# Performance work log

Measured on AMD Instinct MI355X. Metric: run time of the kernel, lower is better.

## Reference

```python
import jax, jax.numpy as jnp
import numpy as np

NEG_SLOPE = 0.2  # PyG GATv2Conv default negative_slope
HEADS1, HID, HEADS2, OUT = 8, 32, 1, 64


def gatv2_layer(x, src, dst, Wl, Wr, att, bias, heads, out_ch, concat):
    """One GATv2Conv (eval mode). x:[N,F], src/dst:[E], Wl/Wr:[F,heads*out_ch], att:[heads,out_ch]."""
    N = x.shape[0]
    xl = (x @ Wl).reshape(N, heads, out_ch)  # source-side transform (lin_l)
    xr = (x @ Wr).reshape(N, heads, out_ch)  # target-side transform (lin_r)
    z = xl[src] + xr[dst]                    # [E, H, C] per-edge pre-activation
    e = jnp.einsum('ehc,hc->eh', jax.nn.leaky_relu(z, NEG_SLOPE), att)  # [E, H]
    # numerically stable edge-softmax segmented by destination node
    m = jax.ops.segment_max(e, dst, num_segments=N)          # [N, H]
    a = jnp.exp(e - m[dst])
    s = jax.ops.segment_sum(a, dst, num_segments=N)          # [N, H]
    alpha = a / s[dst]                                       # [E, H]
    out = jax.ops.segment_sum(alpha[:, :, None] * xl[src], dst, num_segments=N)  # [N, H, C]
    out = out.reshape(N, heads * out_ch) if concat else out.mean(axis=1)
    return out + bias


def setup_inputs() -> dict:
    key = jax.random.key(0)
    ks = jax.random.split(key, 12)
    N, E, F_IN = 50000, 800000, 128
    x = jax.random.normal(ks[0], (N, F_IN), dtype=jnp.float32)
    edge_index = jax.random.randint(ks[1], (2, E), 0, N, dtype=jnp.int32)
    edge_type = jax.random.randint(ks[2], (E,), 0, 5, dtype=jnp.int32)
    sc = 0.05
    Wl1 = jax.random.normal(ks[3], (F_IN, HEADS1 * HID), dtype=jnp.float32) * sc
    Wr1 = jax.random.normal(ks[4], (F_IN, HEADS1 * HID), dtype=jnp.float32) * sc
    att1 = jax.random.normal(ks[5], (HEADS1, HID), dtype=jnp.float32) * sc
    b1 = jnp.zeros((HEADS1 * HID,), dtype=jnp.float32)
    Wl2 = jax.random.normal(ks[6], (HEADS1 * HID, HEADS2 * OUT), dtype=jnp.float32) * sc
    Wr2 = jax.random.normal(ks[7], (HEADS1 * HID, HEADS2 * OUT), dtype=jnp.float32) * sc
    att2 = jax.random.normal(ks[8], (HEADS2, OUT), dtype=jnp.float32) * sc
    b2 = jnp.zeros((OUT,), dtype=jnp.float32)
    return {"x": x, "edge_index": edge_index, "edge_type": edge_type,
            "Wl1": Wl1, "Wr1": Wr1, "att1": att1, "b1": b1,
            "Wl2": Wl2, "Wr2": Wr2, "att2": att2, "b2": b2}


def reference(x, edge_index, edge_type, Wl1, Wr1, att1, b1, Wl2, Wr2, att2, b2):
    # eval mode: F.dropout is identity; edge_type is unused by the original forward
    N = x.shape[0]
    loop = jnp.arange(N, dtype=edge_index.dtype)  # add_self_loops=True (PyG default)
    src = jnp.concatenate([edge_index[0], loop])
    dst = jnp.concatenate([edge_index[1], loop])
    h = jax.nn.elu(gatv2_layer(x, src, dst, Wl1, Wr1, att1, b1, HEADS1, HID, True))
    return gatv2_layer(h, src, dst, Wl2, Wr2, att2, b2, HEADS2, OUT, False)
```

## Files before the change

kernel.cpp:

```cpp
#include <hip/hip_runtime.h>
#include <math.h>

__device__ __forceinline__ float elu1(float z)  { return z > 0.f ? z : (__expf(z) - 1.f); }

__device__ __forceinline__ ushort f2b(float f) {
    uint u = __float_as_uint(f);
    uint r = (u + 0x7FFFu + ((u >> 16) & 1u)) >> 16;
    return (ushort)r;
}
__device__ __forceinline__ float b2f(ushort h) { return __uint_as_float(((uint)h) << 16); }
__device__ __forceinline__ float b2f_lo(uint u) { return __uint_as_float(u << 16); }
__device__ __forceinline__ float b2f_hi(uint u) { return __uint_as_float(u & 0xFFFF0000u); }

typedef __attribute__((ext_vector_type(8))) short short8b;
typedef __attribute__((ext_vector_type(4))) float f32x4;
typedef __attribute__((ext_vector_type(2))) float floatx2;

#define SCAN_BPB 1024


__global__ void k_hist(const int* __restrict__ ei, int E, int Et, int* __restrict__ deg) {
    int i = blockIdx.x * blockDim.x + threadIdx.x;
    if (i < Et) {
        int d = (i < E) ? ei[E + i] : (i - E);
        atomicAdd(&deg[d], 1);
    }
}


__global__ __launch_bounds__(256) void k_scan1(const int* __restrict__ deg, int N,
                                               int* __restrict__ bsum) {
    __shared__ int ts[256];
    int b = blockIdx.x, tid = threadIdx.x;
    int base = b * SCAN_BPB + tid * 4;
    int s = 0;
    if (base + 3 < N) {
        int4 v = *(const int4*)(deg + base);
        s = v.x + v.y + v.z + v.w;
    } else {
        for (int i = 0; i < 4; i++) if (base + i < N) s += deg[base + i];
    }
    ts[tid] = s;
    __syncthreads();
    for (int ofs = 128; ofs > 0; ofs >>= 1) {
        if (tid < ofs) ts[tid] += ts[tid + ofs];
        __syncthreads();
    }
    if (tid == 0) bsum[b] = ts[0];
}

__global__ __launch_bounds__(256) void k_scan2(int* __restrict__ bsum, int nb,
                                               int* __restrict__ offsets, int N) {
    __shared__ int sums[256];
    int tid = threadIdx.x;
    int v = (tid < nb) ? bsum[tid] : 0;
    sums[tid] = v;
    __syncthreads();
    for (int ofs = 1; ofs < 256; ofs <<= 1) {
        int t = 0;
        if (tid >= ofs) t = sums[tid - ofs];
        __syncthreads();
        sums[tid] += t;
        __syncthreads();
    }
    if (tid < nb) bsum[tid] = sums[tid] - v;
    if (tid == 255) offsets[N] = sums[255];
}

__global__ __launch_bounds__(256) void k_scan3(const int* __restrict__ deg, int N,
                                               const int* __restrict__ bsum,
                                               int* __restrict__ offsets,
                                               int* __restrict__ cursor) {
    __shared__ int ts[256];
    int b = blockIdx.x, tid = threadIdx.x;
    int base = b * SCAN_BPB + tid * 4;
    int v[4];
    int s = 0;
#pragma unroll
    for (int i = 0; i < 4; i++) {
        v[i] = (base + i < N) ? deg[base + i] : 0;
        s += v[i];
    }
    ts[tid] = s;
    __syncthreads();
    for (int ofs = 1; ofs < 256; ofs <<= 1) {
        int t = 0;
        if (tid >= ofs) t = ts[tid - ofs];
        __syncthreads();
        ts[tid] += t;
        __syncthreads();
    }
    int run = bsum[b] + ts[tid] - s;
#pragma unroll
    for (int i = 0; i < 4; i++) {
        if (base + i < N) {
            offsets[base + i] = run;
            cursor[base + i]  = run;
        }
        run += v[i];
    }
}

__global__ void k_scatter(const int* __restrict__ ei, int E, int Et,
                          int* __restrict__ cursor, int* __restrict__ srcs) {
    int i = blockIdx.x * blockDim.x + threadIdx.x;
    if (i < Et) {
        int d = (i < E) ? ei[E + i] : (i - E);
        int s = (i < E) ? ei[i]     : (i - E);
        int pos = atomicAdd(&cursor[d], 1);
        srcs[pos] = s;
    }
}


__global__ __launch_bounds__(256) void k_prep(
        const float* __restrict__ Wl1, const float* __restrict__ Wr1,
        ushort* __restrict__ wt1h,
        const float* __restrict__ Wl2, const float* __restrict__ Wr2,
        ushort* __restrict__ wt2h,
        const float* __restrict__ x, ushort* __restrict__ xh,
        int total4) {
    int i = blockIdx.x * blockDim.x + threadIdx.x;
    if (i < 65536) {
        int c = i >> 7, k = i & 127;
        float v = (c < 256) ? Wl1[k * 256 + c] : Wr1[k * 256 + (c - 256)];
        wt1h[i] = f2b(v);
    } else if (i < 98304) {
        int j = i - 65536;
        int c = j >> 8, k = j & 255;
        float v = (c < 64) ? Wl2[k * 64 + c] : Wr2[k * 64 + (c - 64)];
        wt2h[j] = f2b(v);
    } else {
        int j = i - 98304;
        if (j < total4) {
            float4 v = ((const float4*)x)[j];
            ushort4 h;
            h.x = f2b(v.x); h.y = f2b(v.y); h.z = f2b(v.z); h.w = f2b(v.w);
            ((ushort4*)xh)[j] = h;
        }
    }
}


template<int K, int HALF>
__global__ __launch_bounds__(256) void k_gemm_mfma(
        const ushort* __restrict__ a_hi, int AS,
        const ushort* __restrict__ wt_hi,
        ushort* __restrict__ out0, ushort* __restrict__ out1, int N, int nrt) {
    constexpr int LDK = K + 8;
    __shared__ ushort w_hi[128 * LDK];

    int tid = threadIdx.x;
    int cg  = blockIdx.y;
    const uint4* gh = (const uint4*)(wt_hi + (size_t)cg * 128 * K);
#pragma unroll
    for (int j = 0; j < (128 * K / 8) / 256; j++) {
        int idx = j * 256 + tid;
        int col = idx / (K / 8), k8 = idx % (K / 8);
        *(uint4*)&w_hi[col * LDK + k8 * 8] = gh[idx];
    }
    __syncthreads();

    int wid  = tid >> 6, lane = tid & 63;
    int wrg  = wid & 1;
    int wcg  = wid >> 1;
    int r16  = lane & 15, kq = lane >> 4;

    int gcol0 = cg * 128 + wcg * 64;
    ushort* dst = (gcol0 < HALF) ? out0 : out1;
    int dcol0 = (gcol0 < HALF) ? gcol0 : gcol0 - HALF;

    for (int rt = blockIdx.x; rt < nrt; rt += gridDim.x) {
        int row0 = rt * 64 + wrg * 32;
        f32x4 acc[2][4];
#pragma unroll
        for (int rh = 0; rh < 2; rh++)
#pragma unroll
            for (int t = 0; t < 4; t++) acc[rh][t] = (f32x4){0.f, 0.f, 0.f, 0.f};

#pragma unroll
        for (int kk = 0; kk < K / 32; kk++) {
            int ko = kk * 32 + kq * 8;
            short8b ah[2];
#pragma unroll
            for (int rh = 0; rh < 2; rh++) {
                int arow = min(row0 + rh * 16 + r16, N - 1);
                ah[rh] = *(const short8b*)(a_hi + (size_t)arow * AS + ko);
            }
#pragma unroll
            for (int t = 0; t < 4; t++) {
                int wcol = wcg * 64 + t * 16 + r16;
                short8b bh = *(const short8b*)&w_hi[wcol * LDK + ko];
#pragma unroll
                for (int rh = 0; rh < 2; rh++)
                    acc[rh][t] = __builtin_amdgcn_mfma_f32_16x16x32_bf16(ah[rh], bh, acc[rh][t], 0, 0, 0);
            }
        }
#pragma unroll
        for (int rh = 0; rh < 2; rh++)
#pragma unroll
            for (int t = 0; t < 4; t++)
#pragma unroll
                for (int r = 0; r < 4; r++) {
                    int row = row0 + rh * 16 + kq * 4 + r;
                    if (row < N)
                        dst[(size_t)row * HALF + dcol0 + t * 16 + r16] = f2b(acc[rh][t][r]);
                }
    }
}


__global__ __launch_bounds__(256) void k_fused1(const int* __restrict__ srcs, int N,
                                                const int* __restrict__ offsets,
                                                const ushort* __restrict__ xl,
                                                const ushort* __restrict__ xr,
                                                const float* __restrict__ att,
                                                const float* __restrict__ b1,
                                                ushort* __restrict__ h1) {
    int wid  = (blockIdx.x * blockDim.x + threadIdx.x) >> 6;
    int lane = threadIdx.x & 63;
    if (wid >= N) return;
    int start = offsets[wid], end = offsets[wid + 1];
    int g = lane >> 5, l5 = lane & 31;
    int c0 = l5 * 8;

    floatx2 xr2[4], a06[4], a04[4], acc2[4];
    {
        uint4 xraw = *(const uint4*)(xr + (size_t)wid * 256 + c0);
        xr2[0] = (floatx2){b2f_lo(xraw.x), b2f_hi(xraw.x)};
        xr2[1] = (floatx2){b2f_lo(xraw.y), b2f_hi(xraw.y)};
        xr2[2] = (floatx2){b2f_lo(xraw.z), b2f_hi(xraw.z)};
        xr2[3] = (floatx2){b2f_lo(xraw.w), b2f_hi(xraw.w)};
    }
    const floatx2* atp = (const floatx2*)(att + c0);
#pragma unroll
    for (int i = 0; i < 4; i++) {
        floatx2 a = atp[i];
        a06[i] = a * 0.6f;
        a04[i] = a * 0.4f;
        acc2[i] = (floatx2){0.f, 0.f};
    }

    float ssum = 0.f;
    const ushort* xlp = xl + c0;
    for (int p0 = start; p0 < end; p0 += 64) {
        int cnt = end - p0; if (cnt > 64) cnt = 64;
        int sidx = (lane < cnt) ? srcs[p0 + lane] : 0;
        for (int j = 0; j < cnt; j += 2) {
            int idx = j + g;
            int s = __shfl(sidx, idx);
            uint4 raw = *(const uint4*)(xlp + (size_t)s * 256);
            floatx2 v[4];
            v[0] = (floatx2){b2f_lo(raw.x), b2f_hi(raw.x)};
            v[1] = (floatx2){b2f_lo(raw.y), b2f_hi(raw.y)};
            v[2] = (floatx2){b2f_lo(raw.z), b2f_hi(raw.z)};
            v[3] = (floatx2){b2f_lo(raw.w), b2f_hi(raw.w)};
            floatx2 e2 = (floatx2){0.f, 0.f};
#pragma unroll
            for (int i = 0; i < 4; i++) {
                floatx2 z = v[i] + xr2[i];
                e2 += z * a06[i];
                e2 += __builtin_elementwise_abs(z) * a04[i];
            }
            float e = e2.x + e2.y;
            e += __shfl_xor(e, 1);
            e += __shfl_xor(e, 2);
            float w = (idx < cnt) ? __expf(e) : 0.f;
            ssum += w;
            floatx2 w2 = (floatx2){w, w};
#pragma unroll
            for (int i = 0; i < 4; i++) acc2[i] += v[i] * w2;
        }
    }
    ssum += __shfl_xor(ssum, 32);
#pragma unroll
    for (int i = 0; i < 4; i++) {
        acc2[i].x += __shfl_xor(acc2[i].x, 32);
        acc2[i].y += __shfl_xor(acc2[i].y, 32);
    }

    if (g == 0) {
        const floatx2* bvp = (const floatx2*)(b1 + c0);
        float inv = 1.f / ssum;
        ushort oh[8];
#pragma unroll
        for (int i = 0; i < 4; i++) {
            floatx2 bv = bvp[i];
            oh[2*i]   = f2b(elu1(acc2[i].x * inv + bv.x));
            oh[2*i+1] = f2b(elu1(acc2[i].y * inv + bv.y));
        }
        *(uint4*)(h1 + (size_t)wid * 256 + c0) = *(uint4*)oh;
    }
}


__global__ __launch_bounds__(256) void k_fused2(const int* __restrict__ srcs, int N,
                                                const int* __restrict__ offsets,
                                                const ushort* __restrict__ xl,
                                                const ushort* __restrict__ xr,
                                                const float* __restrict__ att,
                                                const float* __restrict__ b2,
                                                float* __restrict__ out) {
    int wid  = (blockIdx.x * blockDim.x + threadIdx.x) >> 6;
    int lane = threadIdx.x & 63;
    if (wid >= N) return;
    int start = offsets[wid], end = offsets[wid + 1];
    int g = lane >> 4, l4 = lane & 15;
    int c0 = l4 * 4;

    floatx2 xr2[2], a06[2], a04[2], acc2[2];
    {
        uint2 xraw = *(const uint2*)(xr + (size_t)wid * 64 + c0);
        xr2[0] = (floatx2){b2f_lo(xraw.x), b2f_hi(xraw.x)};
        xr2[1] = (floatx2){b2f_lo(xraw.y), b2f_hi(xraw.y)};
    }
    const floatx2* atp = (const floatx2*)(att + c0);
#pragma unroll
    for (int i = 0; i < 2; i++) {
        floatx2 a = atp[i];
        a06[i] = a * 0.6f;
        a04[i] = a * 0.4f;
        acc2[i] = (floatx2){0.f, 0.f};
    }

    float ssum = 0.f;
    const ushort* xlp = xl + c0;
    for (int p0 = start; p0 < end; p0 += 64) {
        int cnt = end - p0; if (cnt > 64) cnt = 64;
        int sidx = (lane < cnt) ? srcs[p0 + lane] : 0;
        for (int j = 0; j < cnt; j += 4) {
            int idx = j + g;
            int s = __shfl(sidx, idx);
            uint2 raw = *(const uint2*)(xlp + (size_t)s * 64);
            floatx2 v[2];
            v[0] = (floatx2){b2f_lo(raw.x), b2f_hi(raw.x)};
            v[1] = (floatx2){b2f_lo(raw.y), b2f_hi(raw.y)};
            floatx2 e2 = (floatx2){0.f, 0.f};
#pragma unroll
            for (int i = 0; i < 2; i++) {
                floatx2 z = v[i] + xr2[i];
                e2 += z * a06[i];
                e2 += __builtin_elementwise_abs(z) * a04[i];
            }
            float e = e2.x + e2.y;
            e += __shfl_xor(e, 1);
            e += __shfl_xor(e, 2);
            e += __shfl_xor(e, 4);
            e += __shfl_xor(e, 8);
            float w = (idx < cnt) ? __expf(e) : 0.f;
            ssum += w;
            floatx2 w2 = (floatx2){w, w};
#pragma unroll
            for (int i = 0; i < 2; i++) acc2[i] += v[i] * w2;
        }
    }
    ssum += __shfl_xor(ssum, 16);
    ssum += __shfl_xor(ssum, 32);
#pragma unroll
    for (int i = 0; i < 2; i++) {
        acc2[i].x += __shfl_xor(acc2[i].x, 16);
        acc2[i].x += __shfl_xor(acc2[i].x, 32);
        acc2[i].y += __shfl_xor(acc2[i].y, 16);
        acc2[i].y += __shfl_xor(acc2[i].y, 32);
    }
    if (g == 0) {
        float4 bv = *(const float4*)(b2 + c0);
        float inv = 1.f / ssum;
        float4 o;
        o.x = acc2[0].x * inv + bv.x;
        o.y = acc2[0].y * inv + bv.y;
        o.z = acc2[1].x * inv + bv.z;
        o.w = acc2[1].y * inv + bv.w;
        *(float4*)(out + (size_t)wid * 64 + c0) = o;
    }
}


extern "C" void kernel_launch(void* const* d_in, const int* in_sizes, int n_in,
                              void* d_out, int out_size, void* d_ws, size_t ws_size,
                              hipStream_t stream) {
    const float* x    = (const float*)d_in[0];
    const int*   ei   = (const int*)d_in[1];
    const float* Wl1  = (const float*)d_in[3];
    const float* Wr1  = (const float*)d_in[4];
    const float* att1 = (const float*)d_in[5];
    const float* b1   = (const float*)d_in[6];
    const float* Wl2  = (const float*)d_in[7];
    const float* Wr2  = (const float*)d_in[8];
    const float* att2 = (const float*)d_in[9];
    const float* b2   = (const float*)d_in[10];
    float* out = (float*)d_out;

    const int N  = in_sizes[0] / 128;
    const int E  = in_sizes[1] / 2;
    const int Et = E + N;
    const int nrt = (N + 63) / 64;
    const int nsb = (N + SCAN_BPB - 1) / SCAN_BPB;

    char* ws = (char*)d_ws;
    size_t off = 0;
    auto alloc = [&](size_t bytes) { size_t o = off; off += (bytes + 255) & ~(size_t)255; return o; };
    size_t o_xl1     = alloc((size_t)N * 256 * 2);
    size_t o_xr1     = alloc((size_t)N * 256 * 2);
    size_t o_h1      = alloc((size_t)N * 256 * 2);
    size_t o_offsets = alloc((size_t)(N + 1) * 4);
    size_t o_deg     = alloc((size_t)N * 4);
    size_t o_cursor  = alloc((size_t)N * 4);
    size_t o_srcs    = alloc((size_t)Et * 4);
    size_t o_bsum    = alloc((size_t)256 * 4);
    size_t o_wt1h    = alloc((size_t)512 * 128 * 2);
    size_t o_wt2h    = alloc((size_t)128 * 256 * 2);
    size_t o_xh      = alloc((size_t)N * 128 * 2);
    size_t o_xl2     = alloc((size_t)N * 64 * 2);
    size_t o_xr2     = alloc((size_t)N * 64 * 2);
    (void)ws_size;

    ushort* xl1     = (ushort*)(ws + o_xl1);
    ushort* xr1     = (ushort*)(ws + o_xr1);
    ushort* h1      = (ushort*)(ws + o_h1);
    int*    offsets = (int*)(ws + o_offsets);
    int*    deg     = (int*)(ws + o_deg);
    int*    cursor  = (int*)(ws + o_cursor);
    int*    srcs    = (int*)(ws + o_srcs);
    int*    bsum    = (int*)(ws + o_bsum);
    ushort* wt1h    = (ushort*)(ws + o_wt1h);
    ushort* wt2h    = (ushort*)(ws + o_wt2h);
    ushort* xh      = (ushort*)(ws + o_xh);
    ushort* xl2     = (ushort*)(ws + o_xl2);
    ushort* xr2     = (ushort*)(ws + o_xr2);

    hipMemsetAsync(deg, 0, (size_t)N * 4, stream);
    int tb = 256;
    k_hist<<<(Et + tb - 1) / tb, tb, 0, stream>>>(ei, E, Et, deg);
    k_scan1<<<nsb, 256, 0, stream>>>(deg, N, bsum);
    k_scan2<<<1, 256, 0, stream>>>(bsum, nsb, offsets, N);
    k_scan3<<<nsb, 256, 0, stream>>>(deg, N, bsum, offsets, cursor);
    k_scatter<<<(Et + tb - 1) / tb, tb, 0, stream>>>(ei, E, Et, cursor, srcs);
    int total4 = N * 128 / 4;
    int prep_items = 98304 + total4;
    k_prep<<<(prep_items + 255) / 256, 256, 0, stream>>>(Wl1, Wr1, wt1h,
                                                         Wl2, Wr2, wt2h,
                                                         x, xh, total4);

    k_gemm_mfma<128, 256><<<dim3(256, 4), 256, 0, stream>>>(xh, 128, wt1h, xl1, xr1, N, nrt);
    k_fused1<<<(N + 3) / 4, 256, 0, stream>>>(srcs, N, offsets, xl1, xr1, att1, b1, h1);

    k_gemm_mfma<256, 64><<<dim3(392, 1), 256, 0, stream>>>(h1, 256, wt2h, xl2, xr2, N, nrt);
    k_fused2<<<(N + 3) / 4, 256, 0, stream>>>(srcs, N, offsets, xl2, xr2, att2, b2, out);
}
```

Before: 253.1 us.

## Store layer-1 source features head-sliced and split aggregation across heads

The first GEMM now writes the lin_l output in a head-major layout ([head][node][32]), so each head's features form a compact 3.2 MB slice. The layer-1 aggregation kernel launches one grid plane per head, and each wave processes 8 edges at a time with 64-byte gathers from that slice. The aim is to improve cache locality of the random source gathers, since each head's working set is far smaller than the full 25.6 MB feature table. In exchange it launches eight times as many waves, re-reads offsets and source indices once per head, and adds extra shuffle reductions.

```diff
diff --git a/kernel.cpp b/kernel.cpp
--- a/kernel.cpp
+++ b/kernel.cpp
@@ -142,7 +142,7 @@
 }
 
 
-template<int K, int HALF>
+template<int K, int HALF, bool HSLICE>
 __global__ __launch_bounds__(256) void k_gemm_mfma(
         const ushort* __restrict__ a_hi, int AS,
         const ushort* __restrict__ wt_hi,
@@ -168,6 +168,7 @@
 
     int gcol0 = cg * 128 + wcg * 64;
     ushort* dst = (gcol0 < HALF) ? out0 : out1;
+    bool slice = HSLICE && (gcol0 < HALF);
     int dcol0 = (gcol0 < HALF) ? gcol0 : gcol0 - HALF;
 
     for (int rt = blockIdx.x; rt < nrt; rt += gridDim.x) {
@@ -199,65 +200,67 @@
 #pragma unroll
         for (int rh = 0; rh < 2; rh++)
 #pragma unroll
-            for (int t = 0; t < 4; t++)
+            for (int t = 0; t < 4; t++) {
+                int col = dcol0 + t * 16 + r16;
+                size_t base = slice ? ((size_t)(col >> 5) * N * 32 + (col & 31))
+                                    : (size_t)col;
+                size_t rstride = slice ? 32 : (size_t)HALF;
 #pragma unroll
                 for (int r = 0; r < 4; r++) {
                     int row = row0 + rh * 16 + kq * 4 + r;
-                    if (row < N)
-                        dst[(size_t)row * HALF + dcol0 + t * 16 + r16] = f2b(acc[rh][t][r]);
+                    if (row < N) dst[base + (size_t)row * rstride] = f2b(acc[rh][t][r]);
                 }
+            }
     }
 }
 
 
 __global__ __launch_bounds__(256) void k_fused1(const int* __restrict__ srcs, int N,
                                                 const int* __restrict__ offsets,
-                                                const ushort* __restrict__ xl,
+                                                const ushort* __restrict__ xlh,
                                                 const ushort* __restrict__ xr,
                                                 const float* __restrict__ att,
                                                 const float* __restrict__ b1,
                                                 ushort* __restrict__ h1) {
-    int wid  = (blockIdx.x * blockDim.x + threadIdx.x) >> 6;
+    int node = (blockIdx.x * blockDim.x + threadIdx.x) >> 6;
     int lane = threadIdx.x & 63;
-    if (wid >= N) return;
-    int start = offsets[wid], end = offsets[wid + 1];
-    int g = lane >> 5, l5 = lane & 31;
-    int c0 = l5 * 8;
-
-    floatx2 xr2[4], a06[4], a04[4], acc2[4];
+    if (node >= N) return;
+    int head = blockIdx.y;
+    int g = lane >> 3, l8 = lane & 7;
+    int c0 = l8 * 4;
+
+    const ushort* xlt = xlh + (size_t)head * N * 32;
+
+    floatx2 xr2[2], a06[2], a04[2], acc2[2];
     {
-        uint4 xraw = *(const uint4*)(xr + (size_t)wid * 256 + c0);
+        uint2 xraw = *(const uint2*)(xr + (size_t)node * 256 + head * 32 + c0);
         xr2[0] = (floatx2){b2f_lo(xraw.x), b2f_hi(xraw.x)};
         xr2[1] = (floatx2){b2f_lo(xraw.y), b2f_hi(xraw.y)};
-        xr2[2] = (floatx2){b2f_lo(xraw.z), b2f_hi(xraw.z)};
-        xr2[3] = (floatx2){b2f_lo(xraw.w), b2f_hi(xraw.w)};
-    }
-    const floatx2* atp = (const floatx2*)(att + c0);
-#pragma unroll
-    for (int i = 0; i < 4; i++) {
+    }
+    const floatx2* atp = (const floatx2*)(att + head * 32 + c0);
+#pragma unroll
+    for (int i = 0; i < 2; i++) {
         floatx2 a = atp[i];
         a06[i] = a * 0.6f;
         a04[i] = a * 0.4f;
         acc2[i] = (floatx2){0.f, 0.f};
     }
 
+    int start = offsets[node], end = offsets[node + 1];
     float ssum = 0.f;
-    const ushort* xlp = xl + c0;
     for (int p0 = start; p0 < end; p0 += 64) {
         int cnt = end - p0; if (cnt > 64) cnt = 64;
         int sidx = (lane < cnt) ? srcs[p0 + lane] : 0;
-        for (int j = 0; j < cnt; j += 2) {
+        for (int j = 0; j < cnt; j += 8) {
             int idx = j + g;
             int s = __shfl(sidx, idx);
-            uint4 raw = *(const uint4*)(xlp + (size_t)s * 256);
-            floatx2 v[4];
+            uint2 raw = *(const uint2*)(xlt + (size_t)s * 32 + c0);
+            floatx2 v[2];
             v[0] = (floatx2){b2f_lo(raw.x), b2f_hi(raw.x)};
             v[1] = (floatx2){b2f_lo(raw.y), b2f_hi(raw.y)};
-            v[2] = (floatx2){b2f_lo(raw.z), b2f_hi(raw.z)};
-            v[3] = (floatx2){b2f_lo(raw.w), b2f_hi(raw.w)};
             floatx2 e2 = (floatx2){0.f, 0.f};
 #pragma unroll
-            for (int i = 0; i < 4; i++) {
+            for (int i = 0; i < 2; i++) {
                 floatx2 z = v[i] + xr2[i];
                 e2 += z * a06[i];
                 e2 += __builtin_elementwise_abs(z) * a04[i];
@@ -265,31 +268,38 @@
             float e = e2.x + e2.y;
             e += __shfl_xor(e, 1);
             e += __shfl_xor(e, 2);
+            e += __shfl_xor(e, 4);
             float w = (idx < cnt) ? __expf(e) : 0.f;
             ssum += w;
             floatx2 w2 = (floatx2){w, w};
 #pragma unroll
-            for (int i = 0; i < 4; i++) acc2[i] += v[i] * w2;
-        }
-    }
+            for (int i = 0; i < 2; i++) acc2[i] += v[i] * w2;
+        }
+    }
+    ssum += __shfl_xor(ssum, 8);
+    ssum += __shfl_xor(ssum, 16);
     ssum += __shfl_xor(ssum, 32);
 #pragma unroll
-    for (int i = 0; i < 4; i++) {
+    for (int i = 0; i < 2; i++) {
+        acc2[i].x += __shfl_xor(acc2[i].x, 8);
+        acc2[i].x += __shfl_xor(acc2[i].x, 16);
         acc2[i].x += __shfl_xor(acc2[i].x, 32);
+        acc2[i].y += __shfl_xor(acc2[i].y, 8);
+        acc2[i].y += __shfl_xor(acc2[i].y, 16);
         acc2[i].y += __shfl_xor(acc2[i].y, 32);
     }
 
     if (g == 0) {
-        const floatx2* bvp = (const floatx2*)(b1 + c0);
+        const floatx2* bvp = (const floatx2*)(b1 + head * 32 + c0);
         float inv = 1.f / ssum;
-        ushort oh[8];
-#pragma unroll
-        for (int i = 0; i < 4; i++) {
+        ushort oh[4];
+#pragma unroll
+        for (int i = 0; i < 2; i++) {
             floatx2 bv = bvp[i];
             oh[2*i]   = f2b(elu1(acc2[i].x * inv + bv.x));
             oh[2*i+1] = f2b(elu1(acc2[i].y * inv + bv.y));
         }
-        *(uint4*)(h1 + (size_t)wid * 256 + c0) = *(uint4*)oh;
+        *(uint2*)(h1 + (size_t)node * 256 + head * 32 + c0) = *(uint2*)oh;
     }
 }
 
@@ -442,9 +452,9 @@
                                                          Wl2, Wr2, wt2h,
                                                          x, xh, total4);
 
-    k_gemm_mfma<128, 256><<<dim3(256, 4), 256, 0, stream>>>(xh, 128, wt1h, xl1, xr1, N, nrt);
-    k_fused1<<<(N + 3) / 4, 256, 0, stream>>>(srcs, N, offsets, xl1, xr1, att1, b1, h1);
-
-    k_gemm_mfma<256, 64><<<dim3(392, 1), 256, 0, stream>>>(h1, 256, wt2h, xl2, xr2, N, nrt);
+    k_gemm_mfma<128, 256, true><<<dim3(256, 4), 256, 0, stream>>>(xh, 128, wt1h, xl1, xr1, N, nrt);
+    k_fused1<<<dim3((N + 3) / 4, 8), 256, 0, stream>>>(srcs, N, offsets, xl1, xr1, att1, b1, h1);
+
+    k_gemm_mfma<256, 64, false><<<dim3(392, 1), 256, 0, stream>>>(h1, 256, wt2h, xl2, xr2, N, nrt);
     k_fused2<<<(N + 3) / 4, 256, 0, stream>>>(srcs, N, offsets, xl2, xr2, att2, b2, out);
 }
```

New measurement: 364.6 us. 1.44x slower.
